# Kernel tuning notes

Measured on AMD Instinct MI355X. Metric: run time of the kernel, lower is better.

Reference implementation:

```python
import jax, jax.numpy as jnp
import numpy as np

B, L, D = 32, 256, 1024
H = 8
DQ = D // H            # 128, dim_q == dim_k
DS = 64                # dim_s
DM = 256               # dim_mlp_s
DF = 4096              # dim_feedforward
EPS = 1e-5


def _layernorm(x, g, b):
    mu = jnp.mean(x, axis=-1, keepdims=True)
    var = jnp.mean(jnp.square(x - mu), axis=-1, keepdims=True)
    return (x - mu) * jax.lax.rsqrt(var + EPS) * g + b


def setup_inputs() -> dict:
    key = jax.random.key(0)
    ks = jax.random.split(key, 20)
    s = 0.02
    inp = {
        'src': jax.random.normal(ks[0], (B, L, D), jnp.float32),
        'sf': jax.random.normal(ks[1], (B, DS), jnp.float32),
        'atten_mask': jax.random.randint(ks[2], (B, L, L), 0, 2, jnp.int32),
        # per-head projections, stacked over heads (in,out layout)
        'qw': jax.random.normal(ks[3], (H, D, DQ), jnp.float32) * s,
        'qb': jnp.zeros((H, DQ), jnp.float32),
        'kw': jax.random.normal(ks[4], (H, D, DQ), jnp.float32) * s,
        'kb': jnp.zeros((H, DQ), jnp.float32),
        'vw': jax.random.normal(ks[5], (H, D, DQ), jnp.float32) * s,
        'vb': jnp.zeros((H, DQ), jnp.float32),
        # per-head bias MLP: dim_s -> dim_mlp_s -> L*L
        'b1w': jax.random.normal(ks[6], (H, DS, DM), jnp.float32) * s,
        'b1b': jnp.zeros((H, DM), jnp.float32),
        'b2w': jax.random.normal(ks[7], (H, DM, L * L), jnp.float32) * s,
        'b2b': jnp.zeros((H, L * L), jnp.float32),
        # output projection
        'ow': jax.random.normal(ks[8], (H * DQ, D), jnp.float32) * s,
        'ob': jnp.zeros((D,), jnp.float32),
        # layernorms
        'ln1_g': jnp.ones((D,), jnp.float32), 'ln1_b': jnp.zeros((D,), jnp.float32),
        'ln2_g': jnp.ones((D,), jnp.float32), 'ln2_b': jnp.zeros((D,), jnp.float32),
        # feed-forward
        'w1': jax.random.normal(ks[9], (D, DF), jnp.float32) * s,
        'bf1': jnp.zeros((DF,), jnp.float32),
        'w2': jax.random.normal(ks[10], (DF, D), jnp.float32) * s,
        'bf2': jnp.zeros((D,), jnp.float32),
    }
    return inp


def reference(src, sf, atten_mask, qw, qb, kw, kb, vw, vb, b1w, b1b, b2w, b2b,
              ow, ob, ln1_g, ln1_b, ln2_g, ln2_b, w1, bf1, w2, bf2):
    mask = atten_mask.astype(bool)                      # (B,L,L)
    # per-head projections: (H,B,L,DQ)
    q = jnp.einsum('bld,hdq->hblq', src, qw) + qb[:, None, None, :]
    k = jnp.einsum('bld,hdq->hblq', src, kw) + kb[:, None, None, :]
    v = jnp.einsum('bld,hdq->hblq', src, vw) + vb[:, None, None, :]
    scale = q.shape[-1] ** 0.5
    scores = jnp.einsum('hblq,hbmq->hblm', q, k) / scale
    # masked_fill with constant 1e-9 (NOT -inf), as in the original
    scores = jnp.where(mask[None], jnp.float32(1e-9), scores)
    # per-head learned bias from side features, added AFTER softmax
    hid = jax.nn.relu(jnp.einsum('bs,hsm->hbm', sf, b1w) + b1b[:, None, :])
    bias = (jnp.einsum('hbm,hmn->hbn', hid, b2w) + b2b[:, None, :]).reshape(H, B, L, L)
    soft = jax.nn.softmax(scores, axis=-1) + bias
    out = jnp.einsum('hblm,hbmv->hblv', soft, v)        # (H,B,L,DQ)
    # faithful to original: each head's result is indexed [0] -> batch element 0
    head0 = out[:, 0]                                   # (H,L,DQ)
    hidden = jnp.transpose(head0, (1, 0, 2)).reshape(L, H * DQ)
    attn = hidden @ ow + ob                             # (L,D), broadcasts over batch
    x = _layernorm(src + attn[None], ln1_g, ln1_b)      # (B,L,D)
    ffn = jax.nn.relu(x @ w1 + bf1) @ w2 + bf2
    return _layernorm(x + ffn, ln2_g, ln2_b)
```

## Files before the change

### kernel.cpp

```cpp
#include <hip/hip_runtime.h>

typedef unsigned short u16;
typedef short s16x8 __attribute__((ext_vector_type(8)));
typedef u16 u16x4 __attribute__((ext_vector_type(4)));
typedef float f32x4 __attribute__((ext_vector_type(4)));

#define B_ 32
#define L_ 256
#define D_ 1024
#define H_ 8
#define DQ_ 128
#define DS_ 64
#define DM_ 256
#define DF_ 4096

__device__ __forceinline__ u16 f2bf(float f) {
  unsigned u = __float_as_uint(f);
  unsigned r = (u + 0x7FFFu + ((u >> 16) & 1u)) >> 16;
  return (u16)r;
}
__device__ __forceinline__ float bf2f(u16 x) {
  return __uint_as_float(((unsigned)x) << 16);
}

__device__ __forceinline__ f32x4 mfma16(s16x8 a, s16x8 b, f32x4 c) {
  return __builtin_amdgcn_mfma_f32_16x16x32_bf16(a, b, c, 0, 0, 0);
}

#define GLDS16(g, l)                                                        \
  __builtin_amdgcn_global_load_lds(                                         \
      (__attribute__((address_space(1))) const void*)(g),                   \
      (__attribute__((address_space(3))) void*)(l), 16, 0, 0)

__device__ __forceinline__ void tile_tr(const float* __restrict__ ip,
                                        u16* __restrict__ op, int K, int N,
                                        int bx, int by, float (*t)[33], int tid) {
  const int tx = tid & 31, ty = tid >> 5;
  const long n0 = (long)bx * 32, k0 = (long)by * 32;
#pragma unroll
  for (int i = 0; i < 4; ++i)
    t[ty + i * 8][tx] = ip[(k0 + ty + i * 8) * (long)N + n0 + tx];
  __syncthreads();
#pragma unroll
  for (int i = 0; i < 4; ++i)
    op[(n0 + ty + i * 8) * (long)K + k0 + tx] = f2bf(t[tx][ty + i * 8]);
}

__global__ __launch_bounds__(256) void prep(
    const float* __restrict__ qw, const float* __restrict__ kw,
    const float* __restrict__ vw, const float* __restrict__ src,
    const float* __restrict__ sf, const float* __restrict__ b1w,
    const float* __restrict__ b1b, u16* __restrict__ qwT, u16* __restrict__ kwT,
    u16* __restrict__ vwT, u16* __restrict__ src0b, float* __restrict__ nzv,
    int* __restrict__ nzi, int* __restrict__ nzcnt) {
  const int b = blockIdx.x;
  const int tid = threadIdx.x;
  __shared__ float t[32][33];
  __shared__ float s_sf[DS_];
  __shared__ int wcnt[4];
  if (b < 3072) {
    const int z = b >> 7, rem = b & 127;
    const int sel = z >> 3, h = z & 7;
    const float* ip = (sel == 0 ? qw : (sel == 1 ? kw : vw)) + (long)h * D_ * DQ_;
    u16* op = (sel == 0 ? qwT : (sel == 1 ? kwT : vwT)) + (long)h * DQ_ * D_;
    tile_tr(ip, op, D_, DQ_, rem & 3, rem >> 2, t, tid);
  } else if (b < 3328) {
    const int rem = b - 3072;
    const int i = (rem * 256 + tid) * 4;
    float4 v = *(const float4*)(src + i);
    u16x4 o = {f2bf(v.x), f2bf(v.y), f2bf(v.z), f2bf(v.w)};
    *(u16x4*)(src0b + i) = o;
  } else {
    const int h = b - 3328;
    if (tid < DS_) s_sf[tid] = sf[tid];
    __syncthreads();
    float a = b1b[h * DM_ + tid];
    const float* wp = b1w + (long)h * DS_ * DM_ + tid;
#pragma unroll 8
    for (int s = 0; s < DS_; ++s) a += s_sf[s] * wp[s * DM_];
    a = fmaxf(a, 0.f);
    const unsigned long long bal = __ballot(a > 0.f);
    const int lane = tid & 63, wv = tid >> 6;
    const int pc = __popcll(bal);
    if (lane == 0) wcnt[wv] = pc;
    __syncthreads();
    int base = 0;
    for (int i = 0; i < wv; ++i) base += wcnt[i];
    const int pos = base + __popcll(bal & ((1ull << lane) - 1ull));
    if (a > 0.f) { nzv[h * DM_ + pos] = a; nzi[h * DM_ + pos] = tid; }
    if (tid == 255) nzcnt[h] = base + pc;
  }
}

__global__ __launch_bounds__(256) void phase2(
    const float* __restrict__ nzv, const int* __restrict__ nzi,
    const int* __restrict__ nzcnt, const float* __restrict__ b2w,
    const float* __restrict__ b2b, float* __restrict__ biasb,
    const u16* __restrict__ src0b, const u16* __restrict__ qwT,
    const u16* __restrict__ kwT, const u16* __restrict__ vwT,
    const float* __restrict__ qb, const float* __restrict__ kb,
    const float* __restrict__ vb, u16* __restrict__ q0, u16* __restrict__ k0,
    u16* __restrict__ v0T, const float* __restrict__ ow,
    const float* __restrict__ w1, const float* __restrict__ w2,
    u16* __restrict__ owT, u16* __restrict__ w1T, u16* __restrict__ w2T) {
  const int b = blockIdx.x;
  const int tid = threadIdx.x;
  __shared__ float sv[DM_];
  __shared__ int si[DM_];
  __shared__ u16 smA[128 * 32];
  __shared__ u16 smB[128 * 32];
  __shared__ float t[32][33];
  if (b < 512) {
    const int h = b >> 6;
    const int n0 = (b & 63) << 10;
    const int nnz = nzcnt[h];
    if (tid < DM_) { sv[tid] = nzv[h * DM_ + tid]; si[tid] = nzi[h * DM_ + tid]; }
    __syncthreads();
    const float* wb = b2w + (long)h * DM_ * 65536 + n0 + tid * 4;
    float4 acc = {0.f, 0.f, 0.f, 0.f};
    int j = 0;
    for (; j + 4 <= nnz; j += 4) {
      const float4 a0 = *(const float4*)(wb + (long)si[j] * 65536);
      const float4 a1 = *(const float4*)(wb + (long)si[j + 1] * 65536);
      const float4 a2 = *(const float4*)(wb + (long)si[j + 2] * 65536);
      const float4 a3 = *(const float4*)(wb + (long)si[j + 3] * 65536);
      const float v0 = sv[j], v1 = sv[j + 1], v2 = sv[j + 2], v3 = sv[j + 3];
      acc.x += v0 * a0.x + v1 * a1.x + v2 * a2.x + v3 * a3.x;
      acc.y += v0 * a0.y + v1 * a1.y + v2 * a2.y + v3 * a3.y;
      acc.z += v0 * a0.z + v1 * a1.z + v2 * a2.z + v3 * a3.z;
      acc.w += v0 * a0.w + v1 * a1.w + v2 * a2.w + v3 * a3.w;
    }
    for (; j < nnz; ++j) {
      const float4 a0 = *(const float4*)(wb + (long)si[j] * 65536);
      const float v0 = sv[j];
      acc.x += v0 * a0.x; acc.y += v0 * a0.y; acc.z += v0 * a0.z; acc.w += v0 * a0.w;
    }
    const float4 bb = *(const float4*)(b2b + (long)h * 65536 + n0 + tid * 4);
    float4 o = {acc.x + bb.x, acc.y + bb.y, acc.z + bb.z, acc.w + bb.w};
    *(float4*)(biasb + (long)h * 65536 + n0 + tid * 4) = o;
  } else if (b < 560) {
    const int r = b - 512;
    const int z = r >> 1, sel = z >> 3, h = z & 7;
    const long tm = (long)(r & 1) * 128;
    const int K = D_;
    const u16* BT = (sel == 0 ? qwT : (sel == 1 ? kwT : vwT)) + (long)h * DQ_ * D_;
    const float* bias = (sel == 0 ? qb : (sel == 1 ? kb : vb)) + h * DQ_;
    const int lane = tid & 63;
    const int wv = tid >> 6;
    const int wr = wv >> 1, wc = wv & 1;
    const u16* ga = src0b + (tm + (tid >> 2)) * (long)K + (tid & 3) * 8;
    const u16* gb = BT + (long)(tid >> 2) * K + (tid & 3) * 8;
    const long rstep = 64L * K;
    u16* la = &smA[tid * 8];
    u16* lb = &smB[tid * 8];
    f32x4 acc[4][4];
#pragma unroll
    for (int m = 0; m < 4; ++m)
#pragma unroll
      for (int n = 0; n < 4; ++n) acc[m][n] = (f32x4){0.f, 0.f, 0.f, 0.f};
    for (int k0_ = 0; k0_ < K; k0_ += 32) {
      GLDS16(ga + k0_, la);
      GLDS16(ga + rstep + k0_, la + 64 * 32);
      GLDS16(gb + k0_, lb);
      GLDS16(gb + rstep + k0_, lb + 64 * 32);
      __syncthreads();
      s16x8 af[4], bf[4];
      const int ka = (lane >> 4) * 8;
      const int ra = wr * 64 + (lane & 15);
      const int rb = wc * 64 + (lane & 15);
#pragma unroll
      for (int m = 0; m < 4; ++m) af[m] = *(const s16x8*)&smA[(ra + m * 16) * 32 + ka];
#pragma unroll
      for (int n = 0; n < 4; ++n) bf[n] = *(const s16x8*)&smB[(rb + n * 16) * 32 + ka];
#pragma unroll
      for (int m = 0; m < 4; ++m)
#pragma unroll
        for (int n = 0; n < 4; ++n) acc[m][n] = mfma16(af[m], bf[n], acc[m][n]);
      __syncthreads();
    }
    const long crow0 = tm + wr * 64 + ((lane >> 4) * 4);
    const long ccol0 = wc * 64 + (lane & 15);
#pragma unroll
    for (int m = 0; m < 4; ++m)
#pragma unroll
      for (int n = 0; n < 4; ++n)
#pragma unroll
        for (int i = 0; i < 4; ++i) {
          const long row = crow0 + m * 16 + i;
          const long col = ccol0 + n * 16;
          const float v = acc[m][n][i] + bias[col];
          if (sel < 2) {
            u16* o = (sel == 0 ? q0 : k0) + (long)h * L_ * DQ_;
            o[row * DQ_ + col] = f2bf(v);
          } else {
            v0T[(long)h * DQ_ * L_ + col * L_ + row] = f2bf(v);
          }
        }
  } else if (b < 1584) {
    const int rem = b - 560;
    tile_tr(ow, owT, D_, D_, rem & 31, rem >> 5, t, tid);
  } else if (b < 5680) {
    const int rem = b - 1584;
    tile_tr(w1, w1T, D_, DF_, rem & 127, rem >> 7, t, tid);
  } else {
    const int rem = b - 5680;
    tile_tr(w2, w2T, DF_, D_, rem & 31, rem >> 5, t, tid);
  }
}

__global__ __launch_bounds__(512) void attnproj(
    const u16* __restrict__ q0, const u16* __restrict__ k0,
    const u16* __restrict__ v0T, const float* __restrict__ biasb,
    const int* __restrict__ mask, const u16* __restrict__ owT,
    const float* __restrict__ ob, float* __restrict__ attnvec) {
  extern __shared__ char alds[];
  const int tid = threadIdx.x;
  const int h = tid >> 6;
  const int lane = tid & 63;
  const int lg = lane >> 4;
  const int ll = lane & 15;
  const int r0 = blockIdx.x * 16;

  const u16* q = q0 + (long)h * L_ * DQ_;
  const u16* k = k0 + (long)h * L_ * DQ_;
  s16x8 aq[4];
#pragma unroll
  for (int kk = 0; kk < 4; ++kk)
    aq[kk] = *(const s16x8*)(q + (long)(r0 + ll) * DQ_ + kk * 32 + lg * 8);
  float sc[16][4];
  const float scale = 0.08838834764831845f;
#pragma unroll
  for (int t = 0; t < 16; ++t) {
    f32x4 a = {0.f, 0.f, 0.f, 0.f};
#pragma unroll
    for (int kk = 0; kk < 4; ++kk) {
      s16x8 bf = *(const s16x8*)(k + (long)(t * 16 + ll) * DQ_ + kk * 32 + lg * 8);
      a = mfma16(aq[kk], bf, a);
    }
#pragma unroll
    for (int i = 0; i < 4; ++i) {
      const int row = r0 + lg * 4 + i;
      const int col = t * 16 + ll;
      float s = a[i] * scale;
      if (mask[row * L_ + col] != 0) s = 1e-9f;
      sc[t][i] = s;
    }
  }
#pragma unroll
  for (int i = 0; i < 4; ++i) {
    float mx = sc[0][i];
#pragma unroll
    for (int t = 1; t < 16; ++t) mx = fmaxf(mx, sc[t][i]);
#pragma unroll
    for (int d = 1; d < 16; d <<= 1) mx = fmaxf(mx, __shfl_xor(mx, d));
    float sum = 0.f;
#pragma unroll
    for (int t = 0; t < 16; ++t) {
      const float e = __expf(sc[t][i] - mx);
      sc[t][i] = e;
      sum += e;
    }
#pragma unroll
    for (int d = 1; d < 16; d <<= 1) sum += __shfl_xor(sum, d);
    const float inv = 1.f / sum;
    const int row = r0 + lg * 4 + i;
#pragma unroll
    for (int t = 0; t < 16; ++t)
      sc[t][i] = sc[t][i] * inv + biasb[(long)h * 65536 + (long)row * 256 + t * 16 + ll];
  }
  char* pbuf = alds + h * 8192;
#pragma unroll
  for (int t = 0; t < 16; ++t)
#pragma unroll
    for (int i = 0; i < 4; ++i) {
      const int lr = lg * 4 + i;
      const int cb = (t * 16 + ll) * 2;
      *(u16*)(pbuf + lr * 512 + (cb ^ ((lr & 7) << 4))) = f2bf(sc[t][i]);
    }
  const u16* v = v0T + (long)h * DQ_ * L_;
  char* hidb = alds + 65536;
#pragma unroll
  for (int kk = 0; kk < 8; ++kk) {
  }
  s16x8 paf[8];
#pragma unroll
  for (int kk = 0; kk < 8; ++kk)
    paf[kk] = *(const s16x8*)(pbuf + ll * 512 + ((kk * 64 + lg * 16) ^ ((ll & 7) << 4)));
#pragma unroll
  for (int n = 0; n < 8; ++n) {
    f32x4 a = {0.f, 0.f, 0.f, 0.f};
#pragma unroll
    for (int kk = 0; kk < 8; ++kk) {
      s16x8 bf = *(const s16x8*)(v + (long)(n * 16 + ll) * 256 + kk * 32 + lg * 8);
      a = mfma16(paf[kk], bf, a);
    }
#pragma unroll
    for (int i = 0; i < 4; ++i) {
      const int lr = lg * 4 + i;
      const int cb = (h * 128 + n * 16 + ll) * 2;
      *(u16*)(hidb + lr * 2048 + (cb ^ ((lr & 7) << 4))) = f2bf(a[i]);
    }
  }
  __syncthreads();
  f32x4 acc[8];
#pragma unroll
  for (int f = 0; f < 8; ++f) acc[f] = (f32x4){0.f, 0.f, 0.f, 0.f};
#pragma unroll 2
  for (int k0_ = 0; k0_ < 1024; k0_ += 32) {
    const s16x8 af = *(const s16x8*)(hidb + ll * 2048 + ((k0_ * 2 + lg * 16) ^ ((ll & 7) << 4)));
#pragma unroll
    for (int f = 0; f < 8; ++f) {
      const s16x8 bf = *(const s16x8*)(owT + (long)(h * 128 + f * 16 + ll) * 1024 + k0_ + lg * 8);
      acc[f] = mfma16(af, bf, acc[f]);
    }
  }
#pragma unroll
  for (int f = 0; f < 8; ++f)
#pragma unroll
    for (int i = 0; i < 4; ++i) {
      const int row = r0 + lg * 4 + i;
      const int col = h * 128 + f * 16 + ll;
      attnvec[(long)row * D_ + col] = acc[f][i] + ob[col];
    }
}

template <int BN, int EPI>
__global__ __launch_bounds__(512, 2) void gemm8p(
    const u16* __restrict__ A, const u16* __restrict__ BT, void* __restrict__ Cv,
    const float* __restrict__ bias, const void* __restrict__ R, int M, int N,
    int K, int ldc) {
  extern __shared__ char lds[];
  constexpr int NR = BN / 64;
  constexpr int NHB = BN / 128;
  constexpr int BUF = 32768 + BN * 128;
  constexpr int WST = (NHB == 2) ? 4 : 2;
  const int tid = threadIdx.x;
  const int lane = tid & 63;
  const int w = tid >> 6;
  const int wr = w >> 2, wc = w & 3;

  const int total = gridDim.x;
  int bid = blockIdx.x;
  int s = ((total & 7) == 0) ? ((bid & 7) * (total >> 3) + (bid >> 3)) : bid;
  const int gn = N / BN;
  const long tm = (long)(s / gn) * 256;
  const long tn = (long)(s % gn) * BN;
  const int NT = K >> 6;

  auto stageA = [&](int half, int t) {
    char* hb = lds + (long)(t & 1) * BUF + half * 16384;
    const u16* g = A + (tm + half * 128) * (long)K + (long)t * 64;
#pragma unroll
    for (int j = 0; j < 2; ++j) {
      const int idx = j * 512 + tid;
      const int r = idx >> 3;
      const int c16 = (idx & 7) ^ (r & 7);
      GLDS16(g + (long)r * K + c16 * 8, hb + idx * 16);
    }
  };
  auto stageB = [&](int half, int t) {
    char* hb = lds + (long)(t & 1) * BUF + 32768 + half * 16384;
    const u16* g = BT + (tn + half * 128) * (long)K + (long)t * 64;
#pragma unroll
    for (int j = 0; j < 2; ++j) {
      const int idx = j * 512 + tid;
      const int r = idx >> 3;
      const int c16 = (idx & 7) ^ (r & 7);
      GLDS16(g + (long)r * K + c16 * 8, hb + idx * 16);
    }
  };

  stageA(0, 0);
  stageA(1, 0);
  stageB(0, 0);
  if (NHB == 2) stageB(1, 0);
  stageB(0, 1);
  if (NHB == 2) stageB(1, 1);
  asm volatile("s_waitcnt vmcnt(%0)" ::"n"(WST) : "memory");
  __builtin_amdgcn_s_barrier();

  f32x4 acc[8][NR];
#pragma unroll
  for (int m = 0; m < 8; ++m)
#pragma unroll
    for (int n = 0; n < NR; ++n) acc[m][n] = (f32x4){0.f, 0.f, 0.f, 0.f};

  const int lk = (lane >> 4) * 16;
  const int lr = lane & 15;

  for (int t = 0; t < NT; ++t) {
    const char* bp = lds + (long)(t & 1) * BUF;
    s16x8 bfr[NR][2];
#pragma unroll
    for (int p = 0; p < 4; ++p) {
      if (p == 0) {
#pragma unroll
        for (int ni = 0; ni < NR; ++ni) {
          const int brow = wc * (BN / 4) + ni * 16 + lr;
#pragma unroll
          for (int ks = 0; ks < 2; ++ks) {
            const int kb = (ks * 64 + lk) ^ ((brow & 7) << 4);
            bfr[ni][ks] = *(const s16x8*)(bp + 32768 + brow * 128 + kb);
          }
        }
      }
      s16x8 afr[2][2];
#pragma unroll
      for (int rI = 0; rI < 2; ++rI) {
        const int arow = wr * 128 + (2 * p + rI) * 16 + lr;
#pragma unroll
        for (int ks = 0; ks < 2; ++ks) {
          const int kb = (ks * 64 + lk) ^ ((arow & 7) << 4);
          afr[rI][ks] = *(const s16x8*)(bp + arow * 128 + kb);
        }
      }
      if (p == 0) { if (t + 1 < NT) stageA(0, t + 1); }
      else if (p == 1) { if (t + 1 < NT) stageA(1, t + 1); }
      else if (p == 2) { if (t + 2 < NT) stageB(0, t + 2); }
      else { if (NHB == 2 && t + 2 < NT) stageB(1, t + 2); }
      __builtin_amdgcn_s_barrier();
      __builtin_amdgcn_s_setprio(1);
#pragma unroll
      for (int rI = 0; rI < 2; ++rI)
#pragma unroll
        for (int ni = 0; ni < NR; ++ni)
#pragma unroll
          for (int ks = 0; ks < 2; ++ks)
            acc[2 * p + rI][ni] = mfma16(afr[rI][ks], bfr[ni][ks], acc[2 * p + rI][ni]);
      __builtin_amdgcn_s_setprio(0);
      if (p == 3) {
        if (t + 2 < NT) {
          asm volatile("s_waitcnt vmcnt(%0)" ::"n"(WST) : "memory");
        } else if (t + 1 < NT) {
          asm volatile("s_waitcnt vmcnt(0)" ::: "memory");
        }
      }
      __builtin_amdgcn_s_barrier();
    }
  }

  const long crow0 = tm + wr * 128 + ((lane >> 4) * 4);
  const long ccol0 = tn + wc * (BN / 4) + lr;
#pragma unroll
  for (int m = 0; m < 8; ++m) {
#pragma unroll
    for (int n = 0; n < NR; ++n) {
#pragma unroll
      for (int i = 0; i < 4; ++i) {
        const long row = crow0 + m * 16 + i;
        const long col = ccol0 + n * 16;
        const float v = acc[m][n][i] + bias[col];
        if constexpr (EPI == 1) {
          ((u16*)Cv)[row * (long)ldc + col] = f2bf(fmaxf(v, 0.f));
        } else {
          const float r = bf2f(((const u16*)R)[row * (long)ldc + col]);
          ((u16*)Cv)[row * (long)ldc + col] = f2bf(v + r);
        }
      }
    }
  }
}

template <int MODE>
__global__ __launch_bounds__(256) void ln_kernel(
    const void* __restrict__ in0v, const float* __restrict__ add1,
    const float* __restrict__ g, const float* __restrict__ bb,
    void* __restrict__ outv) {
  const int tid = threadIdx.x;
  const long row = blockIdx.x;
  float4 v;
  if constexpr (MODE == 0) {
    v = ((const float4*)((const float*)in0v + row * D_))[tid];
    const float4 u = ((const float4*)(add1 + (row & (L_ - 1)) * D_))[tid];
    v.x += u.x; v.y += u.y; v.z += u.z; v.w += u.w;
  } else {
    const uint2 pk = *(const uint2*)((const u16*)in0v + row * D_ + tid * 4);
    v.x = __uint_as_float((pk.x & 0xFFFFu) << 16);
    v.y = __uint_as_float(pk.x & 0xFFFF0000u);
    v.z = __uint_as_float((pk.y & 0xFFFFu) << 16);
    v.w = __uint_as_float(pk.y & 0xFFFF0000u);
  }
  float s = v.x + v.y + v.z + v.w;
  float q = v.x * v.x + v.y * v.y + v.z * v.z + v.w * v.w;
#pragma unroll
  for (int d = 1; d < 64; d <<= 1) { s += __shfl_xor(s, d); q += __shfl_xor(q, d); }
  __shared__ float ss[4], sq[4];
  const int wv = tid >> 6;
  if ((tid & 63) == 0) { ss[wv] = s; sq[wv] = q; }
  __syncthreads();
  s = ss[0] + ss[1] + ss[2] + ss[3];
  q = sq[0] + sq[1] + sq[2] + sq[3];
  const float mu = s * (1.f / D_);
  const float var = q * (1.f / D_) - mu * mu;
  const float rs = rsqrtf(var + 1e-5f);
  const float4 gv = ((const float4*)g)[tid];
  const float4 bv = ((const float4*)bb)[tid];
  float4 o;
  o.x = (v.x - mu) * rs * gv.x + bv.x;
  o.y = (v.y - mu) * rs * gv.y + bv.y;
  o.z = (v.z - mu) * rs * gv.z + bv.z;
  o.w = (v.w - mu) * rs * gv.w + bv.w;
  if constexpr (MODE == 0) {
    uint2 pk;
    pk.x = (unsigned)f2bf(o.x) | ((unsigned)f2bf(o.y) << 16);
    pk.y = (unsigned)f2bf(o.z) | ((unsigned)f2bf(o.w) << 16);
    *(uint2*)((u16*)outv + row * D_ + tid * 4) = pk;
  } else {
    ((float4*)((float*)outv + row * D_))[tid] = o;
  }
}

extern "C" void kernel_launch(void* const* d_in, const int* in_sizes, int n_in,
                              void* d_out, int out_size, void* d_ws, size_t ws_size,
                              hipStream_t stream) {
  (void)in_sizes; (void)n_in; (void)out_size; (void)ws_size;
  const float* src = (const float*)d_in[0];
  const float* sf = (const float*)d_in[1];
  const int* mask = (const int*)d_in[2];
  const float* qw = (const float*)d_in[3];
  const float* qb = (const float*)d_in[4];
  const float* kw = (const float*)d_in[5];
  const float* kb = (const float*)d_in[6];
  const float* vw = (const float*)d_in[7];
  const float* vb = (const float*)d_in[8];
  const float* b1w = (const float*)d_in[9];
  const float* b1b = (const float*)d_in[10];
  const float* b2w = (const float*)d_in[11];
  const float* b2b = (const float*)d_in[12];
  const float* ow = (const float*)d_in[13];
  const float* ob = (const float*)d_in[14];
  const float* ln1g = (const float*)d_in[15];
  const float* ln1b = (const float*)d_in[16];
  const float* ln2g = (const float*)d_in[17];
  const float* ln2b = (const float*)d_in[18];
  const float* w1 = (const float*)d_in[19];
  const float* bf1 = (const float*)d_in[20];
  const float* w2 = (const float*)d_in[21];
  const float* bf2 = (const float*)d_in[22];
  float* out = (float*)d_out;

  char* ws = (char*)d_ws;
  size_t off = 0;
  auto alloc = [&](size_t bytes) {
    void* p = ws + off;
    off += (bytes + 255) & ~(size_t)255;
    return p;
  };
  u16* qwT = (u16*)alloc((size_t)H_ * DQ_ * D_ * 2);
  u16* kwT = (u16*)alloc((size_t)H_ * DQ_ * D_ * 2);
  u16* vwT = (u16*)alloc((size_t)H_ * DQ_ * D_ * 2);
  u16* owT = (u16*)alloc((size_t)D_ * D_ * 2);
  u16* w1T = (u16*)alloc((size_t)DF_ * D_ * 2);
  u16* w2T = (u16*)alloc((size_t)D_ * DF_ * 2);
  u16* src0b = (u16*)alloc((size_t)L_ * D_ * 2);
  u16* q0 = (u16*)alloc((size_t)H_ * L_ * DQ_ * 2);
  u16* k0 = (u16*)alloc((size_t)H_ * L_ * DQ_ * 2);
  u16* v0T = (u16*)alloc((size_t)H_ * DQ_ * L_ * 2);
  float* nzv = (float*)alloc((size_t)H_ * DM_ * 4);
  int* nzi = (int*)alloc((size_t)H_ * DM_ * 4);
  int* nzcnt = (int*)alloc(256);
  float* biasb = (float*)alloc((size_t)H_ * L_ * L_ * 4);
  float* attnvec = (float*)alloc((size_t)L_ * D_ * 4);
  u16* xb = (u16*)alloc((size_t)B_ * L_ * D_ * 2);
  u16* ffnh = (u16*)alloc((size_t)B_ * L_ * DF_ * 2);
  u16* yb = (u16*)alloc((size_t)B_ * L_ * D_ * 2);

  hipFuncSetAttribute((const void*)gemm8p<256, 1>,
                      hipFuncAttributeMaxDynamicSharedMemorySize, 131072);
  hipFuncSetAttribute((const void*)gemm8p<128, 2>,
                      hipFuncAttributeMaxDynamicSharedMemorySize, 98304);
  hipFuncSetAttribute((const void*)attnproj,
                      hipFuncAttributeMaxDynamicSharedMemorySize, 98304);

  const dim3 b256(256);
  prep<<<dim3(3336), b256, 0, stream>>>(qw, kw, vw, src, sf, b1w, b1b, qwT, kwT,
                                        vwT, src0b, nzv, nzi, nzcnt);
  phase2<<<dim3(9776), b256, 0, stream>>>(nzv, nzi, nzcnt, b2w, b2b, biasb, src0b,
                                          qwT, kwT, vwT, qb, kb, vb, q0, k0, v0T,
                                          ow, w1, w2, owT, w1T, w2T);
  attnproj<<<dim3(16), dim3(512), 98304, stream>>>(q0, k0, v0T, biasb, mask, owT,
                                                   ob, attnvec);
  ln_kernel<0><<<dim3(B_ * L_), b256, 0, stream>>>(src, attnvec, ln1g, ln1b, xb);
  gemm8p<256, 1><<<dim3(512), dim3(512), 131072, stream>>>(
      xb, w1T, ffnh, bf1, nullptr, B_ * L_, DF_, D_, DF_);
  gemm8p<128, 2><<<dim3(256), dim3(512), 98304, stream>>>(
      ffnh, w2T, yb, bf2, xb, B_ * L_, D_, DF_, D_);
  ln_kernel<1><<<dim3(B_ * L_), b256, 0, stream>>>(yb, nullptr, ln2g, ln2b, out);
}
```

Baseline: 356.5 us.

## Merge prep into phase2 and split attention from output projection

Removes the prep kernel. Each bias block now recomputes the first-layer MLP hidden activations and their nonzero list locally in shared memory. The QKV projection blocks convert src and the weights from fp32 to bf16 on the fly while staging into LDS, instead of reading pre-transposed copies. The fused attention-plus-output-projection kernel is split into a per-head attention kernel that writes a bf16 hidden buffer and a separate tiled GEMM for the output projection. This cuts one launch and the transposed-weight round trip, and gives more parallel blocks to the attention and projection work. In exchange it adds an extra hidden-buffer write and read plus scalar transposing LDS stores.

```diff
diff --git a/kernel.cpp b/kernel.cpp
--- a/kernel.cpp
+++ b/kernel.cpp
@@ -46,32 +46,30 @@
     op[(n0 + ty + i * 8) * (long)K + k0 + tx] = f2bf(t[tx][ty + i * 8]);
 }
 
-__global__ __launch_bounds__(256) void prep(
-    const float* __restrict__ qw, const float* __restrict__ kw,
-    const float* __restrict__ vw, const float* __restrict__ src,
+__global__ __launch_bounds__(256) void mega1(
     const float* __restrict__ sf, const float* __restrict__ b1w,
-    const float* __restrict__ b1b, u16* __restrict__ qwT, u16* __restrict__ kwT,
-    u16* __restrict__ vwT, u16* __restrict__ src0b, float* __restrict__ nzv,
-    int* __restrict__ nzi, int* __restrict__ nzcnt) {
+    const float* __restrict__ b1b, const float* __restrict__ b2w,
+    const float* __restrict__ b2b, float* __restrict__ biasb,
+    const float* __restrict__ src, const float* __restrict__ qw,
+    const float* __restrict__ kw, const float* __restrict__ vw,
+    const float* __restrict__ qb, const float* __restrict__ kb,
+    const float* __restrict__ vb, u16* __restrict__ q0, u16* __restrict__ k0,
+    u16* __restrict__ v0T, const float* __restrict__ ow,
+    const float* __restrict__ w1, const float* __restrict__ w2,
+    u16* __restrict__ owT, u16* __restrict__ w1T, u16* __restrict__ w2T) {
   const int b = blockIdx.x;
   const int tid = threadIdx.x;
-  __shared__ float t[32][33];
   __shared__ float s_sf[DS_];
   __shared__ int wcnt[4];
-  if (b < 3072) {
-    const int z = b >> 7, rem = b & 127;
-    const int sel = z >> 3, h = z & 7;
-    const float* ip = (sel == 0 ? qw : (sel == 1 ? kw : vw)) + (long)h * D_ * DQ_;
-    u16* op = (sel == 0 ? qwT : (sel == 1 ? kwT : vwT)) + (long)h * DQ_ * D_;
-    tile_tr(ip, op, D_, DQ_, rem & 3, rem >> 2, t, tid);
-  } else if (b < 3328) {
-    const int rem = b - 3072;
-    const int i = (rem * 256 + tid) * 4;
-    float4 v = *(const float4*)(src + i);
-    u16x4 o = {f2bf(v.x), f2bf(v.y), f2bf(v.z), f2bf(v.w)};
-    *(u16x4*)(src0b + i) = o;
-  } else {
-    const int h = b - 3328;
+  __shared__ float sv[DM_];
+  __shared__ int si[DM_];
+  __shared__ int snnz;
+  __shared__ u16 smA[128 * 32];
+  __shared__ u16 smB[128 * 40];
+  __shared__ float t[32][33];
+  if (b < 512) {
+    const int h = b >> 6;
+    const int n0 = (b & 63) << 10;
     if (tid < DS_) s_sf[tid] = sf[tid];
     __syncthreads();
     float a = b1b[h * DM_ + tid];
@@ -87,35 +85,10 @@
     int base = 0;
     for (int i = 0; i < wv; ++i) base += wcnt[i];
     const int pos = base + __popcll(bal & ((1ull << lane) - 1ull));
-    if (a > 0.f) { nzv[h * DM_ + pos] = a; nzi[h * DM_ + pos] = tid; }
-    if (tid == 255) nzcnt[h] = base + pc;
-  }
-}
-
-__global__ __launch_bounds__(256) void phase2(
-    const float* __restrict__ nzv, const int* __restrict__ nzi,
-    const int* __restrict__ nzcnt, const float* __restrict__ b2w,
-    const float* __restrict__ b2b, float* __restrict__ biasb,
-    const u16* __restrict__ src0b, const u16* __restrict__ qwT,
-    const u16* __restrict__ kwT, const u16* __restrict__ vwT,
-    const float* __restrict__ qb, const float* __restrict__ kb,
-    const float* __restrict__ vb, u16* __restrict__ q0, u16* __restrict__ k0,
-    u16* __restrict__ v0T, const float* __restrict__ ow,
-    const float* __restrict__ w1, const float* __restrict__ w2,
-    u16* __restrict__ owT, u16* __restrict__ w1T, u16* __restrict__ w2T) {
-  const int b = blockIdx.x;
-  const int tid = threadIdx.x;
-  __shared__ float sv[DM_];
-  __shared__ int si[DM_];
-  __shared__ u16 smA[128 * 32];
-  __shared__ u16 smB[128 * 32];
-  __shared__ float t[32][33];
-  if (b < 512) {
-    const int h = b >> 6;
-    const int n0 = (b & 63) << 10;
-    const int nnz = nzcnt[h];
-    if (tid < DM_) { sv[tid] = nzv[h * DM_ + tid]; si[tid] = nzi[h * DM_ + tid]; }
+    if (a > 0.f) { sv[pos] = a; si[pos] = tid; }
+    if (tid == 255) snnz = base + pc;
     __syncthreads();
+    const int nnz = snnz;
     const float* wb = b2w + (long)h * DM_ * 65536 + n0 + tid * 4;
     float4 acc = {0.f, 0.f, 0.f, 0.f};
     int j = 0;
@@ -142,27 +115,35 @@
     const int r = b - 512;
     const int z = r >> 1, sel = z >> 3, h = z & 7;
     const long tm = (long)(r & 1) * 128;
-    const int K = D_;
-    const u16* BT = (sel == 0 ? qwT : (sel == 1 ? kwT : vwT)) + (long)h * DQ_ * D_;
+    const float* wsrc = (sel == 0 ? qw : (sel == 1 ? kw : vw)) + (long)h * D_ * DQ_;
     const float* bias = (sel == 0 ? qb : (sel == 1 ? kb : vb)) + h * DQ_;
     const int lane = tid & 63;
     const int wv = tid >> 6;
     const int wr = wv >> 1, wc = wv & 1;
-    const u16* ga = src0b + (tm + (tid >> 2)) * (long)K + (tid & 3) * 8;
-    const u16* gb = BT + (long)(tid >> 2) * K + (tid & 3) * 8;
-    const long rstep = 64L * K;
-    u16* la = &smA[tid * 8];
-    u16* lb = &smB[tid * 8];
     f32x4 acc[4][4];
 #pragma unroll
     for (int m = 0; m < 4; ++m)
 #pragma unroll
       for (int n = 0; n < 4; ++n) acc[m][n] = (f32x4){0.f, 0.f, 0.f, 0.f};
-    for (int k0_ = 0; k0_ < K; k0_ += 32) {
-      GLDS16(ga + k0_, la);
-      GLDS16(ga + rstep + k0_, la + 64 * 32);
-      GLDS16(gb + k0_, lb);
-      GLDS16(gb + rstep + k0_, lb + 64 * 32);
+    for (int k0_ = 0; k0_ < D_; k0_ += 32) {
+#pragma unroll
+      for (int jj = 0; jj < 4; ++jj) {
+        const int f4 = jj * 256 + tid;
+        const int row = f4 >> 3, c4 = f4 & 7;
+        const float4 v = *(const float4*)(src + (tm + row) * (long)D_ + k0_ + c4 * 4);
+        u16x4 o = {f2bf(v.x), f2bf(v.y), f2bf(v.z), f2bf(v.w)};
+        *(u16x4*)(&smA[row * 32 + c4 * 4]) = o;
+      }
+#pragma unroll
+      for (int jj = 0; jj < 4; ++jj) {
+        const int f4 = jj * 256 + tid;
+        const int krow = f4 >> 5, n4 = f4 & 31;
+        const float4 v = *(const float4*)(wsrc + (k0_ + krow) * (long)DQ_ + n4 * 4);
+        smB[(n4 * 4 + 0) * 40 + krow] = f2bf(v.x);
+        smB[(n4 * 4 + 1) * 40 + krow] = f2bf(v.y);
+        smB[(n4 * 4 + 2) * 40 + krow] = f2bf(v.z);
+        smB[(n4 * 4 + 3) * 40 + krow] = f2bf(v.w);
+      }
       __syncthreads();
       s16x8 af[4], bf[4];
       const int ka = (lane >> 4) * 8;
@@ -171,7 +152,7 @@
 #pragma unroll
       for (int m = 0; m < 4; ++m) af[m] = *(const s16x8*)&smA[(ra + m * 16) * 32 + ka];
 #pragma unroll
-      for (int n = 0; n < 4; ++n) bf[n] = *(const s16x8*)&smB[(rb + n * 16) * 32 + ka];
+      for (int n = 0; n < 4; ++n) bf[n] = *(const s16x8*)&smB[(rb + n * 16) * 40 + ka];
 #pragma unroll
       for (int m = 0; m < 4; ++m)
 #pragma unroll
@@ -208,21 +189,20 @@
   }
 }
 
-__global__ __launch_bounds__(512) void attnproj(
+__global__ __launch_bounds__(64) void attn_kernel(
     const u16* __restrict__ q0, const u16* __restrict__ k0,
     const u16* __restrict__ v0T, const float* __restrict__ biasb,
-    const int* __restrict__ mask, const u16* __restrict__ owT,
-    const float* __restrict__ ob, float* __restrict__ attnvec) {
-  extern __shared__ char alds[];
-  const int tid = threadIdx.x;
-  const int h = tid >> 6;
-  const int lane = tid & 63;
+    const int* __restrict__ mask, u16* __restrict__ hidden) {
+  __shared__ char pbuf[8192];
+  const int lane = threadIdx.x;
+  const int h = blockIdx.y;
+  const int r0 = blockIdx.x * 16;
   const int lg = lane >> 4;
   const int ll = lane & 15;
-  const int r0 = blockIdx.x * 16;
-
   const u16* q = q0 + (long)h * L_ * DQ_;
   const u16* k = k0 + (long)h * L_ * DQ_;
+  const u16* v = v0T + (long)h * DQ_ * L_;
+
   s16x8 aq[4];
 #pragma unroll
   for (int kk = 0; kk < 4; ++kk)
@@ -268,7 +248,6 @@
     for (int t = 0; t < 16; ++t)
       sc[t][i] = sc[t][i] * inv + biasb[(long)h * 65536 + (long)row * 256 + t * 16 + ll];
   }
-  char* pbuf = alds + h * 8192;
 #pragma unroll
   for (int t = 0; t < 16; ++t)
 #pragma unroll
@@ -277,11 +256,6 @@
       const int cb = (t * 16 + ll) * 2;
       *(u16*)(pbuf + lr * 512 + (cb ^ ((lr & 7) << 4))) = f2bf(sc[t][i]);
     }
-  const u16* v = v0T + (long)h * DQ_ * L_;
-  char* hidb = alds + 65536;
-#pragma unroll
-  for (int kk = 0; kk < 8; ++kk) {
-  }
   s16x8 paf[8];
 #pragma unroll
   for (int kk = 0; kk < 8; ++kk)
@@ -296,32 +270,77 @@
     }
 #pragma unroll
     for (int i = 0; i < 4; ++i) {
-      const int lr = lg * 4 + i;
-      const int cb = (h * 128 + n * 16 + ll) * 2;
-      *(u16*)(hidb + lr * 2048 + (cb ^ ((lr & 7) << 4))) = f2bf(a[i]);
-    }
-  }
-  __syncthreads();
-  f32x4 acc[8];
-#pragma unroll
-  for (int f = 0; f < 8; ++f) acc[f] = (f32x4){0.f, 0.f, 0.f, 0.f};
-#pragma unroll 2
-  for (int k0_ = 0; k0_ < 1024; k0_ += 32) {
-    const s16x8 af = *(const s16x8*)(hidb + ll * 2048 + ((k0_ * 2 + lg * 16) ^ ((ll & 7) << 4)));
-#pragma unroll
-    for (int f = 0; f < 8; ++f) {
-      const s16x8 bf = *(const s16x8*)(owT + (long)(h * 128 + f * 16 + ll) * 1024 + k0_ + lg * 8);
-      acc[f] = mfma16(af, bf, acc[f]);
-    }
-  }
-#pragma unroll
-  for (int f = 0; f < 8; ++f)
-#pragma unroll
-    for (int i = 0; i < 4; ++i) {
       const int row = r0 + lg * 4 + i;
-      const int col = h * 128 + f * 16 + ll;
-      attnvec[(long)row * D_ + col] = acc[f][i] + ob[col];
-    }
+      const int col = n * 16 + ll;
+      hidden[(long)row * 1024 + h * 128 + col] = f2bf(a[i]);
+    }
+  }
+}
+
+__device__ __forceinline__ void g128_core(const u16* __restrict__ A,
+                                          const u16* __restrict__ BT, int K,
+                                          u16* smA, u16* smB,
+                                          f32x4 (&acc)[4][4]) {
+  const int tid = threadIdx.x;
+  const int lane = tid & 63;
+  const int wv = tid >> 6;
+  const int wr = wv >> 1, wc = wv & 1;
+  const u16* ga = A + (long)(tid >> 2) * K + (tid & 3) * 8;
+  const u16* gb = BT + (long)(tid >> 2) * K + (tid & 3) * 8;
+  const long rstep = 64L * K;
+  u16* la = &smA[tid * 8];
+  u16* lb = &smB[tid * 8];
+#pragma unroll
+  for (int m = 0; m < 4; ++m)
+#pragma unroll
+    for (int n = 0; n < 4; ++n) acc[m][n] = (f32x4){0.f, 0.f, 0.f, 0.f};
+  for (int k0 = 0; k0 < K; k0 += 32) {
+    GLDS16(ga + k0, la);
+    GLDS16(ga + rstep + k0, la + 64 * 32);
+    GLDS16(gb + k0, lb);
+    GLDS16(gb + rstep + k0, lb + 64 * 32);
+    __syncthreads();
+    s16x8 af[4], bf[4];
+    const int ka = (lane >> 4) * 8;
+    const int ra = wr * 64 + (lane & 15);
+    const int rb = wc * 64 + (lane & 15);
+#pragma unroll
+    for (int m = 0; m < 4; ++m) af[m] = *(const s16x8*)&smA[(ra + m * 16) * 32 + ka];
+#pragma unroll
+    for (int n = 0; n < 4; ++n) bf[n] = *(const s16x8*)&smB[(rb + n * 16) * 32 + ka];
+#pragma unroll
+    for (int m = 0; m < 4; ++m)
+#pragma unroll
+      for (int n = 0; n < 4; ++n) acc[m][n] = mfma16(af[m], bf[n], acc[m][n]);
+    __syncthreads();
+  }
+}
+
+__global__ __launch_bounds__(256) void gemm_bt(
+    const u16* __restrict__ A, const u16* __restrict__ BT, float* __restrict__ C,
+    const float* __restrict__ bias, int K, int ldc) {
+  __shared__ u16 smA[128 * 32];
+  __shared__ u16 smB[128 * 32];
+  const int tid = threadIdx.x;
+  const long tm = (long)blockIdx.x * 128;
+  const long tn = (long)blockIdx.y * 128;
+  f32x4 acc[4][4];
+  g128_core(A + tm * K, BT + tn * K, K, smA, smB, acc);
+  const int lane = tid & 63;
+  const int wv = tid >> 6;
+  const int wr = wv >> 1, wc = wv & 1;
+  const long crow0 = tm + wr * 64 + ((lane >> 4) * 4);
+  const long ccol0 = tn + wc * 64 + (lane & 15);
+#pragma unroll
+  for (int m = 0; m < 4; ++m)
+#pragma unroll
+    for (int n = 0; n < 4; ++n)
+#pragma unroll
+      for (int i = 0; i < 4; ++i) {
+        const long row = crow0 + m * 16 + i;
+        const long col = ccol0 + n * 16;
+        C[row * (long)ldc + col] = acc[m][n][i] + bias[col];
+      }
 }
 
 template <int BN, int EPI>
@@ -546,20 +565,14 @@
     off += (bytes + 255) & ~(size_t)255;
     return p;
   };
-  u16* qwT = (u16*)alloc((size_t)H_ * DQ_ * D_ * 2);
-  u16* kwT = (u16*)alloc((size_t)H_ * DQ_ * D_ * 2);
-  u16* vwT = (u16*)alloc((size_t)H_ * DQ_ * D_ * 2);
   u16* owT = (u16*)alloc((size_t)D_ * D_ * 2);
   u16* w1T = (u16*)alloc((size_t)DF_ * D_ * 2);
   u16* w2T = (u16*)alloc((size_t)D_ * DF_ * 2);
-  u16* src0b = (u16*)alloc((size_t)L_ * D_ * 2);
   u16* q0 = (u16*)alloc((size_t)H_ * L_ * DQ_ * 2);
   u16* k0 = (u16*)alloc((size_t)H_ * L_ * DQ_ * 2);
   u16* v0T = (u16*)alloc((size_t)H_ * DQ_ * L_ * 2);
-  float* nzv = (float*)alloc((size_t)H_ * DM_ * 4);
-  int* nzi = (int*)alloc((size_t)H_ * DM_ * 4);
-  int* nzcnt = (int*)alloc(256);
   float* biasb = (float*)alloc((size_t)H_ * L_ * L_ * 4);
+  u16* hidden = (u16*)alloc((size_t)L_ * D_ * 2);
   float* attnvec = (float*)alloc((size_t)L_ * D_ * 4);
   u16* xb = (u16*)alloc((size_t)B_ * L_ * D_ * 2);
   u16* ffnh = (u16*)alloc((size_t)B_ * L_ * DF_ * 2);
@@ -569,17 +582,14 @@
                       hipFuncAttributeMaxDynamicSharedMemorySize, 131072);
   hipFuncSetAttribute((const void*)gemm8p<128, 2>,
                       hipFuncAttributeMaxDynamicSharedMemorySize, 98304);
-  hipFuncSetAttribute((const void*)attnproj,
-                      hipFuncAttributeMaxDynamicSharedMemorySize, 98304);
 
   const dim3 b256(256);
-  prep<<<dim3(3336), b256, 0, stream>>>(qw, kw, vw, src, sf, b1w, b1b, qwT, kwT,
-                                        vwT, src0b, nzv, nzi, nzcnt);
-  phase2<<<dim3(9776), b256, 0, stream>>>(nzv, nzi, nzcnt, b2w, b2b, biasb, src0b,
-                                          qwT, kwT, vwT, qb, kb, vb, q0, k0, v0T,
-                                          ow, w1, w2, owT, w1T, w2T);
-  attnproj<<<dim3(16), dim3(512), 98304, stream>>>(q0, k0, v0T, biasb, mask, owT,
-                                                   ob, attnvec);
+  mega1<<<dim3(9776), b256, 0, stream>>>(sf, b1w, b1b, b2w, b2b, biasb, src, qw,
+                                         kw, vw, qb, kb, vb, q0, k0, v0T, ow, w1,
+                                         w2, owT, w1T, w2T);
+  attn_kernel<<<dim3(16, H_), dim3(64), 0, stream>>>(q0, k0, v0T, biasb, mask,
+                                                     hidden);
+  gemm_bt<<<dim3(2, 8), b256, 0, stream>>>(hidden, owT, attnvec, ob, D_, D_);
   ln_kernel<0><<<dim3(B_ * L_), b256, 0, stream>>>(src, attnvec, ln1g, ln1b, xb);
   gemm8p<256, 1><<<dim3(512), dim3(512), 131072, stream>>>(
       xb, w1T, ffnh, bf1, nullptr, B_ * L_, DF_, D_, DF_);
```

Result: no change. 358.5 us (+0.6%).

## Rebalance prep/phase2 work, fuse bias MLP layer-1 into phase2, widen transpose tiles

Applied to the files above, without the earlier changes.

Moves all weight transposes (ow, w1, w2) from phase2 into prep and uses 64x32 transpose tiles with packed 32-bit bf16 stores. Each bias block now recomputes the first bias-MLP layer and its nonzero compaction in shared memory instead of reading it back from global buffers written by prep. The aim is to shorten the serialized phase2 launch, which gates attention, and to cut global round trips and store count. The trade-off is that the small hidden-layer dot products are recomputed redundantly in 512 blocks.

```diff
diff --git a/kernel.cpp b/kernel.cpp
--- a/kernel.cpp
+++ b/kernel.cpp
@@ -32,46 +32,82 @@
       (__attribute__((address_space(1))) const void*)(g),                   \
       (__attribute__((address_space(3))) void*)(l), 16, 0, 0)
 
-__device__ __forceinline__ void tile_tr(const float* __restrict__ ip,
-                                        u16* __restrict__ op, int K, int N,
-                                        int bx, int by, float (*t)[33], int tid) {
+__device__ __forceinline__ void tile_tr64(const float* __restrict__ ip,
+                                          u16* __restrict__ op, int K, int N,
+                                          int bx, int by, float (*t)[33],
+                                          int tid) {
   const int tx = tid & 31, ty = tid >> 5;
-  const long n0 = (long)bx * 32, k0 = (long)by * 32;
-#pragma unroll
-  for (int i = 0; i < 4; ++i)
+  const long n0 = (long)bx * 32, k0 = (long)by * 64;
+#pragma unroll
+  for (int i = 0; i < 8; ++i)
     t[ty + i * 8][tx] = ip[(k0 + ty + i * 8) * (long)N + n0 + tx];
   __syncthreads();
-#pragma unroll
-  for (int i = 0; i < 4; ++i)
-    op[(n0 + ty + i * 8) * (long)K + k0 + tx] = f2bf(t[tx][ty + i * 8]);
+  const int c2 = tid & 31;
+  const int r8 = tid >> 5;
+#pragma unroll
+  for (int i = 0; i < 4; ++i) {
+    const int n = r8 + i * 8;
+    const unsigned lo = (unsigned)f2bf(t[c2 * 2][n]);
+    const unsigned hi = (unsigned)f2bf(t[c2 * 2 + 1][n]);
+    *(unsigned*)(&op[(n0 + n) * (long)K + k0 + c2 * 2]) = lo | (hi << 16);
+  }
 }
 
 __global__ __launch_bounds__(256) void prep(
     const float* __restrict__ qw, const float* __restrict__ kw,
     const float* __restrict__ vw, const float* __restrict__ src,
-    const float* __restrict__ sf, const float* __restrict__ b1w,
-    const float* __restrict__ b1b, u16* __restrict__ qwT, u16* __restrict__ kwT,
-    u16* __restrict__ vwT, u16* __restrict__ src0b, float* __restrict__ nzv,
-    int* __restrict__ nzi, int* __restrict__ nzcnt) {
+    const float* __restrict__ ow, const float* __restrict__ w1,
+    const float* __restrict__ w2, u16* __restrict__ qwT, u16* __restrict__ kwT,
+    u16* __restrict__ vwT, u16* __restrict__ src0b, u16* __restrict__ owT,
+    u16* __restrict__ w1T, u16* __restrict__ w2T) {
   const int b = blockIdx.x;
   const int tid = threadIdx.x;
-  __shared__ float t[32][33];
-  __shared__ float s_sf[DS_];
-  __shared__ int wcnt[4];
-  if (b < 3072) {
-    const int z = b >> 7, rem = b & 127;
+  __shared__ float t[64][33];
+  if (b < 1536) {
+    const int z = b >> 6, rem = b & 63;
     const int sel = z >> 3, h = z & 7;
     const float* ip = (sel == 0 ? qw : (sel == 1 ? kw : vw)) + (long)h * D_ * DQ_;
     u16* op = (sel == 0 ? qwT : (sel == 1 ? kwT : vwT)) + (long)h * DQ_ * D_;
-    tile_tr(ip, op, D_, DQ_, rem & 3, rem >> 2, t, tid);
-  } else if (b < 3328) {
-    const int rem = b - 3072;
+    tile_tr64(ip, op, D_, DQ_, rem & 3, rem >> 2, t, tid);
+  } else if (b < 1792) {
+    const int rem = b - 1536;
     const int i = (rem * 256 + tid) * 4;
     float4 v = *(const float4*)(src + i);
     u16x4 o = {f2bf(v.x), f2bf(v.y), f2bf(v.z), f2bf(v.w)};
     *(u16x4*)(src0b + i) = o;
+  } else if (b < 2304) {
+    const int rem = b - 1792;
+    tile_tr64(ow, owT, D_, D_, rem & 31, rem >> 5, t, tid);
+  } else if (b < 4352) {
+    const int rem = b - 2304;
+    tile_tr64(w1, w1T, D_, DF_, rem & 127, rem >> 7, t, tid);
   } else {
-    const int h = b - 3328;
+    const int rem = b - 4352;
+    tile_tr64(w2, w2T, DF_, D_, rem & 31, rem >> 5, t, tid);
+  }
+}
+
+__global__ __launch_bounds__(256) void phase2(
+    const float* __restrict__ sf, const float* __restrict__ b1w,
+    const float* __restrict__ b1b, const float* __restrict__ b2w,
+    const float* __restrict__ b2b, float* __restrict__ biasb,
+    const u16* __restrict__ src0b, const u16* __restrict__ qwT,
+    const u16* __restrict__ kwT, const u16* __restrict__ vwT,
+    const float* __restrict__ qb, const float* __restrict__ kb,
+    const float* __restrict__ vb, u16* __restrict__ q0, u16* __restrict__ k0,
+    u16* __restrict__ v0T) {
+  const int b = blockIdx.x;
+  const int tid = threadIdx.x;
+  __shared__ float s_sf[DS_];
+  __shared__ int wcnt[4];
+  __shared__ float sv[DM_];
+  __shared__ int si[DM_];
+  __shared__ int snnz;
+  __shared__ u16 smA[128 * 32];
+  __shared__ u16 smB[128 * 32];
+  if (b < 512) {
+    const int h = b >> 6;
+    const int n0 = (b & 63) << 10;
     if (tid < DS_) s_sf[tid] = sf[tid];
     __syncthreads();
     float a = b1b[h * DM_ + tid];
@@ -87,35 +123,10 @@
     int base = 0;
     for (int i = 0; i < wv; ++i) base += wcnt[i];
     const int pos = base + __popcll(bal & ((1ull << lane) - 1ull));
-    if (a > 0.f) { nzv[h * DM_ + pos] = a; nzi[h * DM_ + pos] = tid; }
-    if (tid == 255) nzcnt[h] = base + pc;
-  }
-}
-
-__global__ __launch_bounds__(256) void phase2(
-    const float* __restrict__ nzv, const int* __restrict__ nzi,
-    const int* __restrict__ nzcnt, const float* __restrict__ b2w,
-    const float* __restrict__ b2b, float* __restrict__ biasb,
-    const u16* __restrict__ src0b, const u16* __restrict__ qwT,
-    const u16* __restrict__ kwT, const u16* __restrict__ vwT,
-    const float* __restrict__ qb, const float* __restrict__ kb,
-    const float* __restrict__ vb, u16* __restrict__ q0, u16* __restrict__ k0,
-    u16* __restrict__ v0T, const float* __restrict__ ow,
-    const float* __restrict__ w1, const float* __restrict__ w2,
-    u16* __restrict__ owT, u16* __restrict__ w1T, u16* __restrict__ w2T) {
-  const int b = blockIdx.x;
-  const int tid = threadIdx.x;
-  __shared__ float sv[DM_];
-  __shared__ int si[DM_];
-  __shared__ u16 smA[128 * 32];
-  __shared__ u16 smB[128 * 32];
-  __shared__ float t[32][33];
-  if (b < 512) {
-    const int h = b >> 6;
-    const int n0 = (b & 63) << 10;
-    const int nnz = nzcnt[h];
-    if (tid < DM_) { sv[tid] = nzv[h * DM_ + tid]; si[tid] = nzi[h * DM_ + tid]; }
+    if (a > 0.f) { sv[pos] = a; si[pos] = tid; }
+    if (tid == 255) snnz = base + pc;
     __syncthreads();
+    const int nnz = snnz;
     const float* wb = b2w + (long)h * DM_ * 65536 + n0 + tid * 4;
     float4 acc = {0.f, 0.f, 0.f, 0.f};
     int j = 0;
@@ -138,7 +149,7 @@
     const float4 bb = *(const float4*)(b2b + (long)h * 65536 + n0 + tid * 4);
     float4 o = {acc.x + bb.x, acc.y + bb.y, acc.z + bb.z, acc.w + bb.w};
     *(float4*)(biasb + (long)h * 65536 + n0 + tid * 4) = o;
-  } else if (b < 560) {
+  } else {
     const int r = b - 512;
     const int z = r >> 1, sel = z >> 3, h = z & 7;
     const long tm = (long)(r & 1) * 128;
@@ -196,15 +207,6 @@
             v0T[(long)h * DQ_ * L_ + col * L_ + row] = f2bf(v);
           }
         }
-  } else if (b < 1584) {
-    const int rem = b - 560;
-    tile_tr(ow, owT, D_, D_, rem & 31, rem >> 5, t, tid);
-  } else if (b < 5680) {
-    const int rem = b - 1584;
-    tile_tr(w1, w1T, D_, DF_, rem & 127, rem >> 7, t, tid);
-  } else {
-    const int rem = b - 5680;
-    tile_tr(w2, w2T, DF_, D_, rem & 31, rem >> 5, t, tid);
   }
 }
 
@@ -279,9 +281,6 @@
     }
   const u16* v = v0T + (long)h * DQ_ * L_;
   char* hidb = alds + 65536;
-#pragma unroll
-  for (int kk = 0; kk < 8; ++kk) {
-  }
   s16x8 paf[8];
 #pragma unroll
   for (int kk = 0; kk < 8; ++kk)
@@ -556,9 +555,6 @@
   u16* q0 = (u16*)alloc((size_t)H_ * L_ * DQ_ * 2);
   u16* k0 = (u16*)alloc((size_t)H_ * L_ * DQ_ * 2);
   u16* v0T = (u16*)alloc((size_t)H_ * DQ_ * L_ * 2);
-  float* nzv = (float*)alloc((size_t)H_ * DM_ * 4);
-  int* nzi = (int*)alloc((size_t)H_ * DM_ * 4);
-  int* nzcnt = (int*)alloc(256);
   float* biasb = (float*)alloc((size_t)H_ * L_ * L_ * 4);
   float* attnvec = (float*)alloc((size_t)L_ * D_ * 4);
   u16* xb = (u16*)alloc((size_t)B_ * L_ * D_ * 2);
@@ -573,11 +569,10 @@
                       hipFuncAttributeMaxDynamicSharedMemorySize, 98304);
 
   const dim3 b256(256);
-  prep<<<dim3(3336), b256, 0, stream>>>(qw, kw, vw, src, sf, b1w, b1b, qwT, kwT,
-                                        vwT, src0b, nzv, nzi, nzcnt);
-  phase2<<<dim3(9776), b256, 0, stream>>>(nzv, nzi, nzcnt, b2w, b2b, biasb, src0b,
-                                          qwT, kwT, vwT, qb, kb, vb, q0, k0, v0T,
-                                          ow, w1, w2, owT, w1T, w2T);
+  prep<<<dim3(6400), b256, 0, stream>>>(qw, kw, vw, src, ow, w1, w2, qwT, kwT,
+                                        vwT, src0b, owT, w1T, w2T);
+  phase2<<<dim3(560), b256, 0, stream>>>(sf, b1w, b1b, b2w, b2b, biasb, src0b,
+                                         qwT, kwT, vwT, qb, kb, vb, q0, k0, v0T);
   attnproj<<<dim3(16), dim3(512), 98304, stream>>>(q0, k0, v0T, biasb, mask, owT,
                                                    ob, attnvec);
   ln_kernel<0><<<dim3(B_ * L_), b256, 0, stream>>>(src, attnvec, ln1g, ln1b, xb);
```

Result: no change. 357.6 us (+0.3%).
